# Kernel tuning notes

Measured on AMD Instinct MI355X. Metric: run time of the kernel, lower is better.

Reference implementation:

```python
import jax, jax.numpy as jnp
import numpy as np

N, E, NC = 50000, 800000, 5
H, C = 4, 16      # branch GATConvs: heads=4, out=16 -> 64
H2, C2 = 4, 32    # conv2/conv3: heads=4, out=32 -> 128
HID = 128


def _gat(x, src, dst, W, a_s, a_d, b, mask=None, edge_attr=None, We=None, a_e=None):
    """PyG-style GATConv with add_self_loops=True (fill_value='mean' for edge_attr)."""
    n = x.shape[0]
    h, c = a_s.shape
    hx = (x @ W).reshape(n, h, c)                      # [N,H,C]
    as_n = (hx * a_s).sum(-1)                          # [N,H]
    ad_n = (hx * a_d).sum(-1)                          # [N,H]
    alpha = as_n[src] + ad_n[dst]                      # [E,H]
    loop = as_n + ad_n                                 # self-loop scores [N,H]
    if edge_attr is not None:
        ee = (edge_attr @ We).reshape(-1, h, c)        # [E,H,C]
        alpha = alpha + (ee * a_e).sum(-1)
        w = mask.astype(x.dtype) if mask is not None else jnp.ones((edge_attr.shape[0],), x.dtype)
        # fill_value='mean': self-loop attr = mean of (masked) incoming edge_attr
        loop_attr = jax.ops.segment_sum(edge_attr * w[:, None], dst, n) / \
                    jnp.maximum(jax.ops.segment_sum(w, dst, n), 1.0)[:, None]
        loop = loop + ((loop_attr @ We).reshape(n, h, c) * a_e).sum(-1)
    alpha = jax.nn.leaky_relu(alpha, 0.2)
    loop = jax.nn.leaky_relu(loop, 0.2)
    if mask is not None:
        alpha = jnp.where(mask[:, None], alpha, -jnp.inf)
    # segment softmax over destination neighborhoods (self-loop always present)
    m = jnp.maximum(jax.ops.segment_max(alpha, dst, n), loop)      # [N,H], finite
    ex = jnp.exp(alpha - m[dst])                                   # [E,H]
    if mask is not None:
        ex = jnp.where(mask[:, None], ex, 0.0)
    exl = jnp.exp(loop - m)                                        # [N,H]
    denom = jax.ops.segment_sum(ex, dst, n) + exl
    out = jax.ops.segment_sum(ex[:, :, None] * hx[src], dst, n) + exl[:, :, None] * hx
    return (out / denom[:, :, None]).reshape(n, h * c) + b


def setup_inputs() -> dict:
    key = jax.random.key(0)
    ks = iter(jax.random.split(key, 64))
    def nrm(shape, s=0.1):
        return jax.random.normal(next(ks), shape, jnp.float32) * s
    d = {}
    d["x"] = nrm((N, 1), 1.0)
    d["edge_index"] = jax.random.randint(next(ks), (2, E), 0, N, jnp.int32)
    d["edge_attr"] = nrm((E, 3), 1.0)
    d["mask_t"] = jax.random.randint(next(ks), (E,), 0, 2, jnp.int32).astype(bool)
    d["mask_g"] = jax.random.randint(next(ks), (E,), 0, 2, jnp.int32).astype(bool)
    d["mask_p"] = jax.random.randint(next(ks), (E,), 0, 2, jnp.int32).astype(bool)
    for p in ("t", "g", "p"):
        d[f"W{p}"] = nrm((1, H * C))
        d[f"a{p}s"] = nrm((H, C)); d[f"a{p}d"] = nrm((H, C)); d[f"a{p}e"] = nrm((H, C))
        d[f"W{p}e"] = nrm((3, H * C))
        d[f"b{p}"] = jnp.zeros((H * C,), jnp.float32)
    d["Wf"] = nrm((3 * H * C, HID)); d["bf"] = jnp.zeros((HID,), jnp.float32)
    d["W2"] = nrm((HID, H2 * C2)); d["a2s"] = nrm((H2, C2)); d["a2d"] = nrm((H2, C2)); d["b2"] = jnp.zeros((H2 * C2,), jnp.float32)
    d["W3"] = nrm((HID, H2 * C2)); d["a3s"] = nrm((H2, C2)); d["a3d"] = nrm((H2, C2)); d["b3"] = jnp.zeros((H2 * C2,), jnp.float32)
    d["Wc1"] = nrm((HID, HID // 2)); d["bc1"] = jnp.zeros((HID // 2,), jnp.float32)
    d["Wc2"] = nrm((HID // 2, NC)); d["bc2"] = jnp.zeros((NC,), jnp.float32)
    return d


def reference(x, edge_index, edge_attr, mask_t, mask_g, mask_p,
              Wt, ats, atd, ate, Wte, bt,
              Wg, ags, agd, age, Wge, bg,
              Wp, aps, apd, ape, Wpe, bp,
              Wf, bf, W2, a2s, a2d, b2, W3, a3s, a3d, b3,
              Wc1, bc1, Wc2, bc2):
    src, dst = edge_index[0], edge_index[1]
    ht = _gat(x, src, dst, Wt, ats, atd, bt, mask_t, edge_attr, Wte, ate)
    hg = _gat(x, src, dst, Wg, ags, agd, bg, mask_g, edge_attr, Wge, age)
    hp = _gat(x, src, dst, Wp, aps, apd, bp, mask_p, edge_attr, Wpe, ape)
    h = jax.nn.relu(jnp.concatenate([ht, hg, hp], -1) @ Wf + bf)
    h = jax.nn.relu(_gat(h, src, dst, W2, a2s, a2d, b2))
    h = jax.nn.relu(_gat(h, src, dst, W3, a3s, a3d, b3))
    logits = jax.nn.relu(h @ Wc1 + bc1) @ Wc2 + bc2
    return jax.nn.log_softmax(logits, -1)
```

## Files before the change

kernel.cpp:

```cpp
#include <hip/hip_runtime.h>
#include <hip/hip_bf16.h>

#define LEAKY(v) ((v) > 0.f ? (v) : 0.2f * (v))

typedef __attribute__((ext_vector_type(8))) short s8;
typedef __attribute__((ext_vector_type(4))) float f4;
typedef __attribute__((ext_vector_type(4))) unsigned short us4;

__device__ __forceinline__ unsigned short f_to_bf16(float f) {
    union { float f; unsigned int i; } v; v.f = f;
    unsigned int x = v.i;
    return (unsigned short)((x + 0x7fffu + ((x >> 16) & 1u)) >> 16);
}

__device__ __forceinline__ float2 bf2_to_f2(unsigned int u) {
    union { unsigned int i; float f; } a, b;
    a.i = (u & 0xffffu) << 16;
    b.i = u & 0xffff0000u;
    float2 r; r.x = a.f; r.y = b.f;
    return r;
}

struct ConstBuf {
    float ws[3][4];
    float wd[3][4];
    float M[3][3][4];
    float G[12][128];
    float bias2[128];
};
#define CB_FLOATS 1724

struct BranchW { const float *W, *as_, *ad_, *ae, *We, *b; };
struct PreArgs { BranchW br[3]; const float *Wf, *bf; ConstBuf* cb; };

__global__ void k_pre_all(PreArgs A, const float* __restrict__ W2, unsigned short* __restrict__ wf2,
                          const float* __restrict__ W3, unsigned short* __restrict__ wf3,
                          int* __restrict__ deg, int N) {
    int t = threadIdx.x;
    if (blockIdx.x == 0) {
        if (t < 24) {
            int b = t / 8, r = t % 8, h = r & 3; bool isd = r >= 4;
            const float* a = isd ? A.br[b].ad_ : A.br[b].as_;
            float s = 0.f;
            for (int c = 0; c < 16; ++c) s += A.br[b].W[h * 16 + c] * a[h * 16 + c];
            if (isd) A.cb->wd[b][h] = s; else A.cb->ws[b][h] = s;
        }
        if (t >= 32 && t < 68) {
            int id = t - 32, b = id / 12, k = (id % 12) / 4, h = id & 3;
            float s = 0.f;
            for (int c = 0; c < 16; ++c) s += A.br[b].We[k * 64 + h * 16 + c] * A.br[b].ae[h * 16 + c];
            A.cb->M[b][k][h] = s;
        }
        if (t >= 128) {
            int j = t - 128;
            float s = A.bf[j];
            for (int b = 0; b < 3; ++b)
                for (int i = 0; i < 64; ++i)
                    s += A.br[b].b[i] * A.Wf[(b * 64 + i) * 128 + j];
            A.cb->bias2[j] = s;
        }
        for (int id = t; id < 1536; id += 256) {
            int r = id >> 7, j = id & 127, b = r >> 2, h = r & 3;
            float s = 0.f;
            for (int c = 0; c < 16; ++c)
                s += A.br[b].W[h * 16 + c] * A.Wf[(b * 64 + h * 16 + c) * 128 + j];
            A.cb->G[r][j] = s;
        }
    } else if (blockIdx.x <= 2) {
        const float* W = (blockIdx.x == 1) ? W2 : W3;
        unsigned short* out = (blockIdx.x == 1) ? wf2 : wf3;
        for (int i = t; i < 16384; i += 256) {
            int j = i & 7, lane = (i >> 3) & 63, kk = (i >> 9) & 3, ct = i >> 11;
            int k = kk * 32 + (lane >> 4) * 8 + j;
            int n = ct * 16 + (lane & 15);
            out[i] = f_to_bf16(W[k * 128 + n]);
        }
    } else {
        int idx = (blockIdx.x - 3) * 256 + t;
        if (idx < N) deg[idx] = 0;
    }
}

__global__ void k_count(const int* __restrict__ ei, int E, int* __restrict__ deg) {
    int e = blockIdx.x * blockDim.x + threadIdx.x;
    if (e < E) atomicAdd(&deg[ei[E + e]], 1);
}

#define SCAN_EPB 2048

__global__ void k_scan1(const int* __restrict__ deg, int* __restrict__ off,
                        int* __restrict__ partials, int total) {
    __shared__ int sd[256];
    int t = threadIdx.x;
    int base = blockIdx.x * SCAN_EPB + t * 8;
    int v[8];
    int s = 0;
    #pragma unroll
    for (int i = 0; i < 8; ++i) {
        int idx = base + i;
        v[i] = (idx < total - 1) ? deg[idx] : 0;
        s += v[i];
    }
    sd[t] = s;
    __syncthreads();
    #pragma unroll
    for (int ofs = 1; ofs < 256; ofs <<= 1) {
        int u = (t >= ofs) ? sd[t - ofs] : 0;
        __syncthreads();
        sd[t] += u;
        __syncthreads();
    }
    if (t == 255) partials[blockIdx.x] = sd[255];
    int run = sd[t] - s;
    #pragma unroll
    for (int i = 0; i < 8; ++i) {
        int idx = base + i;
        if (idx < total) off[idx] = run;
        run += v[i];
    }
}

__global__ void k_scan3(int* __restrict__ off, const int* __restrict__ partials,
                        int* __restrict__ cursor, int total) {
    int idx = blockIdx.x * blockDim.x + threadIdx.x;
    if (idx < total) {
        int pb = idx / SCAN_EPB;
        int addv = 0;
        for (int j = 0; j < pb; ++j) addv += partials[j];
        int v = off[idx] + addv;
        off[idx] = v;
        if (idx < total - 1) cursor[idx] = v;
    }
}

__global__ void k_scatter(const int* __restrict__ ei, const float* __restrict__ attr,
                          const int* __restrict__ mt, const int* __restrict__ mg,
                          const int* __restrict__ mp, int E, int chunk,
                          int* __restrict__ cursor, float4* __restrict__ rec) {
    int r = blockIdx.x & 7;
    int slice = blockIdx.x >> 3;
    int e = slice * 256 + threadIdx.x;
    if (e >= E) return;
    int d = ei[E + e];
    if ((unsigned)(d - r * chunk) >= (unsigned)chunk) return;
    int p = atomicAdd(&cursor[d], 1);
    float4 rr;
    rr.x = attr[e * 3 + 0];
    rr.y = attr[e * 3 + 1];
    rr.z = attr[e * 3 + 2];
    unsigned int bits = (mt[e] != 0 ? 1u : 0u) | (mg[e] != 0 ? 2u : 0u) | (mp[e] != 0 ? 4u : 0u);
    rr.w = __int_as_float((int)((unsigned)ei[e] | (bits << 16)));
    rec[p] = rr;
}

__global__ void k_branch(const float* __restrict__ x, const int* __restrict__ off,
                         const float4* __restrict__ rec, int* __restrict__ csr_src,
                         const ConstBuf* __restrict__ cb, float* __restrict__ h1, int N) {
    __shared__ float sc[CB_FLOATS];
    for (int i = threadIdx.x; i < CB_FLOATS; i += 256) sc[i] = ((const float*)cb)[i];
    __syncthreads();
    int g = threadIdx.x >> 4, l = threadIdx.x & 15;
    int n = blockIdx.x * 16 + g;
    if (n >= N) return;

    float num[12], den[12], asum[9], cnt[3];
    #pragma unroll
    for (int i = 0; i < 12; ++i) { num[i] = 0.f; den[i] = 0.f; }
    #pragma unroll
    for (int i = 0; i < 9; ++i) asum[i] = 0.f;
    cnt[0] = cnt[1] = cnt[2] = 0.f;

    float xn = x[n];
    int beg = off[n], end = off[n + 1];
    for (int p = beg + l; p < end; p += 16) {
        float4 r = rec[p];
        unsigned int packed = (unsigned int)__float_as_int(r.w);
        int src = (int)(packed & 0xffffu);
        unsigned int bits = packed >> 16;
        csr_src[p] = src;
        float xs = x[src];
        float a0 = r.x, a1 = r.y, a2 = r.z;
        #pragma unroll
        for (int b = 0; b < 3; ++b) {
            if ((bits >> b) & 1u) {
                cnt[b] += 1.f;
                asum[b * 3 + 0] += a0; asum[b * 3 + 1] += a1; asum[b * 3 + 2] += a2;
                #pragma unroll
                for (int h = 0; h < 4; ++h) {
                    float al = xs * sc[b * 4 + h] + xn * sc[12 + b * 4 + h]
                             + a0 * sc[24 + b * 12 + 0 + h]
                             + a1 * sc[24 + b * 12 + 4 + h]
                             + a2 * sc[24 + b * 12 + 8 + h];
                    al = LEAKY(al);
                    float ex = __expf(al);
                    den[b * 4 + h] += ex;
                    num[b * 4 + h] += ex * xs;
                }
            }
        }
    }
    #pragma unroll
    for (int m = 1; m < 16; m <<= 1) {
        #pragma unroll
        for (int i = 0; i < 12; ++i) {
            num[i] += __shfl_xor(num[i], m, 64);
            den[i] += __shfl_xor(den[i], m, 64);
        }
        #pragma unroll
        for (int i = 0; i < 9; ++i) asum[i] += __shfl_xor(asum[i], m, 64);
        #pragma unroll
        for (int i = 0; i < 3; ++i) cnt[i] += __shfl_xor(cnt[i], m, 64);
    }
    float S[12];
    #pragma unroll
    for (int b = 0; b < 3; ++b) {
        float inv = 1.f / fmaxf(cnt[b], 1.f);
        float l0 = asum[b * 3 + 0] * inv, l1 = asum[b * 3 + 1] * inv, l2 = asum[b * 3 + 2] * inv;
        #pragma unroll
        for (int h = 0; h < 4; ++h) {
            float lp = xn * (sc[b * 4 + h] + sc[12 + b * 4 + h])
                     + l0 * sc[24 + b * 12 + 0 + h]
                     + l1 * sc[24 + b * 12 + 4 + h]
                     + l2 * sc[24 + b * 12 + 8 + h];
            lp = LEAKY(lp);
            float exl = __expf(lp);
            float sden = den[b * 4 + h] + exl;
            S[b * 4 + h] = (num[b * 4 + h] + exl * xn) / sden;
        }
    }
    int jb = l * 8;
    float o[8];
    #pragma unroll
    for (int q = 0; q < 8; ++q) {
        int j = jb + q;
        float a = sc[60 + 1536 + j];
        #pragma unroll
        for (int k = 0; k < 12; ++k) a += S[k] * sc[60 + k * 128 + j];
        o[q] = fmaxf(a, 0.f);
    }
    float4* dst = (float4*)(h1 + (size_t)n * 128 + jb);
    dst[0] = make_float4(o[0], o[1], o[2], o[3]);
    dst[1] = make_float4(o[4], o[5], o[6], o[7]);
}

__global__ void k_mm128b(const float* __restrict__ A, const unsigned short* __restrict__ wf,
                         const float* __restrict__ a_s, const float* __restrict__ a_d,
                         unsigned short* __restrict__ hxb, float* __restrict__ as_,
                         float* __restrict__ ad_, int N) {
    __shared__ unsigned short sA[64 * 136];
    __shared__ unsigned short sW[16384];
    int tid = threadIdx.x;
    int base = blockIdx.x * 64;
    const float4* wf4 = (const float4*)wf;
    float4* sW4 = (float4*)sW;
    #pragma unroll
    for (int i = 0; i < 8; ++i) sW4[tid + i * 256] = wf4[tid + i * 256];
    #pragma unroll
    for (int i = 0; i < 8; ++i) {
        int f = tid + i * 256;
        int row = f >> 5, c4 = f & 31;
        int n = base + row;
        float4 v = (n < N) ? ((const float4*)A)[(size_t)n * 32 + c4]
                           : make_float4(0.f, 0.f, 0.f, 0.f);
        us4 b;
        b.x = f_to_bf16(v.x); b.y = f_to_bf16(v.y);
        b.z = f_to_bf16(v.z); b.w = f_to_bf16(v.w);
        *(us4*)(&sA[row * 136 + c4 * 4]) = b;
    }
    __syncthreads();
    int wv = tid >> 6, lane = tid & 63;
    int q = lane >> 4, l15 = lane & 15;
    int rowbase = wv * 16;
    s8 af[4];
    #pragma unroll
    for (int kk = 0; kk < 4; ++kk)
        af[kk] = *(const s8*)(&sA[(rowbase + l15) * 136 + kk * 32 + q * 8]);
    float as8[8], ad8[8];
    #pragma unroll
    for (int ct = 0; ct < 8; ++ct) { as8[ct] = a_s[ct * 16 + l15]; ad8[ct] = a_d[ct * 16 + l15]; }
    float ss[4][4], sdd[4][4];
    #pragma unroll
    for (int r = 0; r < 4; ++r)
        #pragma unroll
        for (int hh = 0; hh < 4; ++hh) { ss[r][hh] = 0.f; sdd[r][hh] = 0.f; }
    #pragma unroll
    for (int ct = 0; ct < 8; ++ct) {
        f4 acc = {0.f, 0.f, 0.f, 0.f};
        #pragma unroll
        for (int kk = 0; kk < 4; ++kk) {
            s8 bfr = *(const s8*)(&sW[((ct * 4 + kk) * 64 + lane) * 8]);
            acc = __builtin_amdgcn_mfma_f32_16x16x32_bf16(af[kk], bfr, acc, 0, 0, 0);
        }
        int hh = ct >> 1;
        float asv = as8[ct], adv = ad8[ct];
        #pragma unroll
        for (int r = 0; r < 4; ++r) {
            int n = base + rowbase + q * 4 + r;
            if (n < N) hxb[(size_t)n * 128 + ct * 16 + l15] = f_to_bf16(acc[r]);
            ss[r][hh] += acc[r] * asv;
            sdd[r][hh] += acc[r] * adv;
        }
    }
    #pragma unroll
    for (int m = 1; m < 16; m <<= 1) {
        #pragma unroll
        for (int r = 0; r < 4; ++r)
            #pragma unroll
            for (int hh = 0; hh < 4; ++hh) {
                ss[r][hh] += __shfl_xor(ss[r][hh], m, 64);
                sdd[r][hh] += __shfl_xor(sdd[r][hh], m, 64);
            }
    }
    #pragma unroll
    for (int hh = 0; hh < 4; ++hh) {
        if (l15 == hh) {
            #pragma unroll
            for (int r = 0; r < 4; ++r) {
                int n = base + rowbase + q * 4 + r;
                if (n < N) {
                    as_[(size_t)n * 4 + hh] = ss[r][hh];
                    ad_[(size_t)n * 4 + hh] = sdd[r][hh];
                }
            }
        }
    }
}

__global__ void k_gatagg(const unsigned short* __restrict__ hxb, const float* __restrict__ as_,
                         const float* __restrict__ ad_, const float* __restrict__ b,
                         const int* __restrict__ off, const int* __restrict__ csr_src,
                         float* __restrict__ out, int N) {
    int wave = threadIdx.x >> 6, lane = threadIdx.x & 63;
    int n = blockIdx.x * 4 + wave;
    if (n >= N) return;
    int h = lane >> 4;
    int lofs = lane * 2;
    int hm = lane & 3;
    int im = lane >> 2;
    float adn = ad_[(size_t)n * 4 + h];
    float adnm = ad_[(size_t)n * 4 + hm];
    int beg = off[n], end = off[n + 1];
    float acc0 = 0.f, acc1 = 0.f, accd = 0.f;
    for (int p = beg; p < end; p += 16) {
        int pm = p + im;
        bool vm = pm < end;
        int sm = csr_src[vm ? pm : beg];
        float em = as_[(size_t)sm * 4 + hm];
        float exm = vm ? __expf(LEAKY(em + adnm)) : 0.f;
        #pragma unroll
        for (int i = 0; i < 16; ++i) {
            int sb = __shfl(sm, i * 4, 64);
            float ex = __shfl(exm, i * 4 + h, 64);
            unsigned int u = *(const unsigned int*)(hxb + (size_t)sb * 128 + lofs);
            float2 v = bf2_to_f2(u);
            acc0 += ex * v.x; acc1 += ex * v.y; accd += ex;
        }
    }
    float aln = LEAKY(as_[(size_t)n * 4 + h] + adn);
    float exl = __expf(aln);
    unsigned int un = *(const unsigned int*)(hxb + (size_t)n * 128 + lofs);
    float2 vn = bf2_to_f2(un);
    float inv = 1.f / (accd + exl);
    float o0 = (acc0 + exl * vn.x) * inv + b[lofs + 0];
    float o1 = (acc1 + exl * vn.y) * inv + b[lofs + 1];
    float2 r; r.x = fmaxf(o0, 0.f); r.y = fmaxf(o1, 0.f);
    *(float2*)(out + (size_t)n * 128 + lofs) = r;
}

#define CLS_NPB 32
__global__ void k_cls(const float* __restrict__ h3, const float* __restrict__ Wc1,
                      const float* __restrict__ bc1, const float* __restrict__ Wc2,
                      const float* __restrict__ bc2, float* __restrict__ out, int N) {
    __shared__ float hs[CLS_NPB * 128];
    int tid = threadIdx.x;
    int nb = blockIdx.x * CLS_NPB;
    for (int i = tid; i < CLS_NPB * 128; i += 256) {
        int n = nb + (i >> 7);
        hs[i] = (n < N) ? h3[(size_t)n * 128 + (i & 127)] : 0.f;
    }
    __syncthreads();
    int g = tid >> 6, j = tid & 63;
    const float4* hb4 = (const float4*)(hs + g * 8 * 128);
    float bj = bc1[j];
    float acc[8];
    #pragma unroll
    for (int i = 0; i < 8; ++i) acc[i] = bj;
    for (int k = 0; k < 128; k += 4) {
        float w0 = Wc1[(k + 0) * 64 + j];
        float w1 = Wc1[(k + 1) * 64 + j];
        float w2 = Wc1[(k + 2) * 64 + j];
        float w3 = Wc1[(k + 3) * 64 + j];
        #pragma unroll
        for (int i = 0; i < 8; ++i) {
            float4 h4 = hb4[(i * 128 + k) >> 2];
            acc[i] += h4.x * w0 + h4.y * w1 + h4.z * w2 + h4.w * w3;
        }
    }
    float w2v[5];
    #pragma unroll
    for (int c = 0; c < 5; ++c) w2v[c] = Wc2[j * 5 + c];
    #pragma unroll
    for (int i = 0; i < 8; ++i) {
        float t = fmaxf(acc[i], 0.f);
        float p[5];
        #pragma unroll
        for (int c = 0; c < 5; ++c) p[c] = t * w2v[c];
        #pragma unroll
        for (int m = 1; m < 64; m <<= 1) {
            #pragma unroll
            for (int c = 0; c < 5; ++c) p[c] += __shfl_xor(p[c], m, 64);
        }
        if (j == 0) {
            int n = nb + g * 8 + i;
            if (n < N) {
                float l[5], mx = -1e30f;
                #pragma unroll
                for (int c = 0; c < 5; ++c) { l[c] = p[c] + bc2[c]; mx = fmaxf(mx, l[c]); }
                float s = 0.f;
                #pragma unroll
                for (int c = 0; c < 5; ++c) s += __expf(l[c] - mx);
                float lse = mx + __logf(s);
                #pragma unroll
                for (int c = 0; c < 5; ++c) out[(size_t)n * 5 + c] = l[c] - lse;
            }
        }
    }
}

extern "C" void kernel_launch(void* const* d_in, const int* in_sizes, int n_in,
                              void* d_out, int out_size, void* d_ws, size_t ws_size,
                              hipStream_t stream) {
    const float* x    = (const float*)d_in[0];
    const int*   ei   = (const int*)d_in[1];
    const float* attr = (const float*)d_in[2];
    const int*   mt   = (const int*)d_in[3];
    const int*   mg   = (const int*)d_in[4];
    const int*   mp   = (const int*)d_in[5];
    const float* Wf   = (const float*)d_in[24];
    const float* bf   = (const float*)d_in[25];
    const float* W2   = (const float*)d_in[26];
    const float* a2s  = (const float*)d_in[27];
    const float* a2d  = (const float*)d_in[28];
    const float* b2   = (const float*)d_in[29];
    const float* W3   = (const float*)d_in[30];
    const float* a3s  = (const float*)d_in[31];
    const float* a3d  = (const float*)d_in[32];
    const float* b3   = (const float*)d_in[33];
    const float* Wc1  = (const float*)d_in[34];
    const float* bc1  = (const float*)d_in[35];
    const float* Wc2  = (const float*)d_in[36];
    const float* bc2  = (const float*)d_in[37];

    int N = in_sizes[0];
    int E = in_sizes[1] / 2;

    char* w = (char*)d_ws;
    auto alloc = [&](size_t bytes) {
        char* p = w;
        w += (bytes + 255) & ~(size_t)255;
        return p;
    };
    int* off      = (int*)alloc((size_t)(N + 1) * 4);
    int* cursor   = (int*)alloc((size_t)N * 4);
    int* deg      = (int*)alloc((size_t)N * 4);
    int* partials = (int*)alloc(1024 * 4);
    int* csr_src  = (int*)alloc((size_t)E * 4);
    ConstBuf* cb  = (ConstBuf*)alloc(sizeof(ConstBuf));
    float* as_    = (float*)alloc((size_t)N * 4 * 4);
    float* ad_    = (float*)alloc((size_t)N * 4 * 4);
    float* bufA   = (float*)alloc((size_t)N * 128 * 4);
    float4* rec   = (float4*)alloc((size_t)E * 16);
    unsigned short* hxb = (unsigned short*)alloc((size_t)N * 256);
    unsigned short* wf2 = (unsigned short*)alloc(16384 * 2);
    unsigned short* wf3 = (unsigned short*)alloc(16384 * 2);

    PreArgs pa;
    for (int b = 0; b < 3; ++b) {
        pa.br[b].W   = (const float*)d_in[6 + b * 6 + 0];
        pa.br[b].as_ = (const float*)d_in[6 + b * 6 + 1];
        pa.br[b].ad_ = (const float*)d_in[6 + b * 6 + 2];
        pa.br[b].ae  = (const float*)d_in[6 + b * 6 + 3];
        pa.br[b].We  = (const float*)d_in[6 + b * 6 + 4];
        pa.br[b].b   = (const float*)d_in[6 + b * 6 + 5];
    }
    pa.Wf = Wf; pa.bf = bf; pa.cb = cb;

    int total = N + 1;
    int nScanBlocks = (total + SCAN_EPB - 1) / SCAN_EPB;

    hipLaunchKernelGGL(k_pre_all, dim3(3 + (N + 255) / 256), dim3(256), 0, stream,
                       pa, W2, wf2, W3, wf3, deg, N);
    int gE = (E + 255) / 256;
    hipLaunchKernelGGL(k_count, dim3(gE), dim3(256), 0, stream, ei, E, deg);
    hipLaunchKernelGGL(k_scan1, dim3(nScanBlocks), dim3(256), 0, stream, deg, off, partials, total);
    hipLaunchKernelGGL(k_scan3, dim3((total + 255) / 256), dim3(256), 0, stream,
                       off, partials, cursor, total);
    int chunk = (N + 7) / 8;
    hipLaunchKernelGGL(k_scatter, dim3(gE * 8), dim3(256), 0, stream,
                       ei, attr, mt, mg, mp, E, chunk, cursor, rec);
    hipLaunchKernelGGL(k_branch, dim3((N + 15) / 16), dim3(256), 0, stream,
                       x, off, rec, csr_src, cb, bufA, N);
    hipLaunchKernelGGL(k_mm128b, dim3((N + 63) / 64), dim3(256), 0, stream,
                       bufA, wf2, a2s, a2d, hxb, as_, ad_, N);
    hipLaunchKernelGGL(k_gatagg, dim3((N + 3) / 4), dim3(256), 0, stream,
                       hxb, as_, ad_, b2, off, csr_src, bufA, N);
    hipLaunchKernelGGL(k_mm128b, dim3((N + 63) / 64), dim3(256), 0, stream,
                       bufA, wf3, a3s, a3d, hxb, as_, ad_, N);
    hipLaunchKernelGGL(k_gatagg, dim3((N + 3) / 4), dim3(256), 0, stream,
                       hxb, as_, ad_, b3, off, csr_src, bufA, N);
    hipLaunchKernelGGL(k_cls, dim3((N + CLS_NPB - 1) / CLS_NPB), dim3(256), 0, stream,
                       bufA, Wc1, bc1, Wc2, bc2, (float*)d_out, N);
}
```

Measured before the change: 438.4 us.

## Store intermediate node features in bf16 and run classifier on MFMA

Intermediate 128-wide node features from the branch, GAT aggregation and classifier input are now written and read as bf16 instead of fp32. This halves their memory traffic and removes the fp32-to-bf16 conversion inside the matmul loader. The classifier's first layer now uses bf16 MFMA with a weight matrix pre-swizzled in the prep kernel, replacing the scalar FMA loop. The cost is lower precision in the stored activations and in the classifier matmul.

Measured after the change: 403.8 us (median of 2 runs). 7.9% less time.

```diff
diff --git a/kernel.cpp b/kernel.cpp
--- a/kernel.cpp
+++ b/kernel.cpp
@@ -35,6 +35,7 @@
 
 __global__ void k_pre_all(PreArgs A, const float* __restrict__ W2, unsigned short* __restrict__ wf2,
                           const float* __restrict__ W3, unsigned short* __restrict__ wf3,
+                          const float* __restrict__ Wc1, unsigned short* __restrict__ wc1f,
                           int* __restrict__ deg, int N) {
     int t = threadIdx.x;
     if (blockIdx.x == 0) {
@@ -75,8 +76,15 @@
             int n = ct * 16 + (lane & 15);
             out[i] = f_to_bf16(W[k * 128 + n]);
         }
+    } else if (blockIdx.x == 3) {
+        for (int i = t; i < 8192; i += 256) {
+            int j = i & 7, lane = (i >> 3) & 63, kk = (i >> 9) & 3, ct = i >> 11;
+            int k = kk * 32 + (lane >> 4) * 8 + j;
+            int col = ct * 16 + (lane & 15);
+            wc1f[i] = f_to_bf16(Wc1[k * 64 + col]);
+        }
     } else {
-        int idx = (blockIdx.x - 3) * 256 + t;
+        int idx = (blockIdx.x - 4) * 256 + t;
         if (idx < N) deg[idx] = 0;
     }
 }
@@ -155,7 +163,7 @@
 
 __global__ void k_branch(const float* __restrict__ x, const int* __restrict__ off,
                          const float4* __restrict__ rec, int* __restrict__ csr_src,
-                         const ConstBuf* __restrict__ cb, float* __restrict__ h1, int N) {
+                         const ConstBuf* __restrict__ cb, unsigned short* __restrict__ h1, int N) {
     __shared__ float sc[CB_FLOATS];
     for (int i = threadIdx.x; i < CB_FLOATS; i += 256) sc[i] = ((const float*)cb)[i];
     __syncthreads();
@@ -229,21 +237,25 @@
         }
     }
     int jb = l * 8;
-    float o[8];
-    #pragma unroll
-    for (int q = 0; q < 8; ++q) {
-        int j = jb + q;
-        float a = sc[60 + 1536 + j];
-        #pragma unroll
-        for (int k = 0; k < 12; ++k) a += S[k] * sc[60 + k * 128 + j];
-        o[q] = fmaxf(a, 0.f);
-    }
-    float4* dst = (float4*)(h1 + (size_t)n * 128 + jb);
-    dst[0] = make_float4(o[0], o[1], o[2], o[3]);
-    dst[1] = make_float4(o[4], o[5], o[6], o[7]);
-}
-
-__global__ void k_mm128b(const float* __restrict__ A, const unsigned short* __restrict__ wf,
+    unsigned int o[4];
+    #pragma unroll
+    for (int q2 = 0; q2 < 4; ++q2) {
+        float v0, v1;
+        #pragma unroll
+        for (int s = 0; s < 2; ++s) {
+            int j = jb + q2 * 2 + s;
+            float a = sc[60 + 1536 + j];
+            #pragma unroll
+            for (int k = 0; k < 12; ++k) a += S[k] * sc[60 + k * 128 + j];
+            if (s == 0) v0 = fmaxf(a, 0.f); else v1 = fmaxf(a, 0.f);
+        }
+        o[q2] = (unsigned int)f_to_bf16(v0) | ((unsigned int)f_to_bf16(v1) << 16);
+    }
+    uint4 pack; pack.x = o[0]; pack.y = o[1]; pack.z = o[2]; pack.w = o[3];
+    *(uint4*)(h1 + (size_t)n * 128 + jb) = pack;
+}
+
+__global__ void k_mm128b(const unsigned short* __restrict__ A, const unsigned short* __restrict__ wf,
                          const float* __restrict__ a_s, const float* __restrict__ a_d,
                          unsigned short* __restrict__ hxb, float* __restrict__ as_,
                          float* __restrict__ ad_, int N) {
@@ -256,16 +268,13 @@
     #pragma unroll
     for (int i = 0; i < 8; ++i) sW4[tid + i * 256] = wf4[tid + i * 256];
     #pragma unroll
-    for (int i = 0; i < 8; ++i) {
+    for (int i = 0; i < 4; ++i) {
         int f = tid + i * 256;
-        int row = f >> 5, c4 = f & 31;
+        int row = f >> 4, c8 = f & 15;
         int n = base + row;
-        float4 v = (n < N) ? ((const float4*)A)[(size_t)n * 32 + c4]
-                           : make_float4(0.f, 0.f, 0.f, 0.f);
-        us4 b;
-        b.x = f_to_bf16(v.x); b.y = f_to_bf16(v.y);
-        b.z = f_to_bf16(v.z); b.w = f_to_bf16(v.w);
-        *(us4*)(&sA[row * 136 + c4 * 4]) = b;
+        uint4 v = (n < N) ? ((const uint4*)A)[(size_t)n * 16 + c8]
+                          : make_uint4(0u, 0u, 0u, 0u);
+        *(uint4*)(&sA[row * 136 + c8 * 8]) = v;
     }
     __syncthreads();
     int wv = tid >> 6, lane = tid & 63;
@@ -329,7 +338,7 @@
 __global__ void k_gatagg(const unsigned short* __restrict__ hxb, const float* __restrict__ as_,
                          const float* __restrict__ ad_, const float* __restrict__ b,
                          const int* __restrict__ off, const int* __restrict__ csr_src,
-                         float* __restrict__ out, int N) {
+                         unsigned short* __restrict__ out, int N) {
     int wave = threadIdx.x >> 6, lane = threadIdx.x & 63;
     int n = blockIdx.x * 4 + wave;
     if (n >= N) return;
@@ -361,68 +370,87 @@
     unsigned int un = *(const unsigned int*)(hxb + (size_t)n * 128 + lofs);
     float2 vn = bf2_to_f2(un);
     float inv = 1.f / (accd + exl);
-    float o0 = (acc0 + exl * vn.x) * inv + b[lofs + 0];
-    float o1 = (acc1 + exl * vn.y) * inv + b[lofs + 1];
-    float2 r; r.x = fmaxf(o0, 0.f); r.y = fmaxf(o1, 0.f);
-    *(float2*)(out + (size_t)n * 128 + lofs) = r;
-}
-
-#define CLS_NPB 32
-__global__ void k_cls(const float* __restrict__ h3, const float* __restrict__ Wc1,
+    float o0 = fmaxf((acc0 + exl * vn.x) * inv + b[lofs + 0], 0.f);
+    float o1 = fmaxf((acc1 + exl * vn.y) * inv + b[lofs + 1], 0.f);
+    unsigned int pk = (unsigned int)f_to_bf16(o0) | ((unsigned int)f_to_bf16(o1) << 16);
+    *(unsigned int*)(out + (size_t)n * 128 + lofs) = pk;
+}
+
+__global__ void k_cls(const unsigned short* __restrict__ h3, const unsigned short* __restrict__ wc1f,
                       const float* __restrict__ bc1, const float* __restrict__ Wc2,
                       const float* __restrict__ bc2, float* __restrict__ out, int N) {
-    __shared__ float hs[CLS_NPB * 128];
+    __shared__ unsigned short sA[64 * 136];
+    __shared__ unsigned short sW[8192];
     int tid = threadIdx.x;
-    int nb = blockIdx.x * CLS_NPB;
-    for (int i = tid; i < CLS_NPB * 128; i += 256) {
-        int n = nb + (i >> 7);
-        hs[i] = (n < N) ? h3[(size_t)n * 128 + (i & 127)] : 0.f;
+    int base = blockIdx.x * 64;
+    const float4* wf4 = (const float4*)wc1f;
+    float4* sW4 = (float4*)sW;
+    #pragma unroll
+    for (int i = 0; i < 4; ++i) sW4[tid + i * 256] = wf4[tid + i * 256];
+    #pragma unroll
+    for (int i = 0; i < 4; ++i) {
+        int f = tid + i * 256;
+        int row = f >> 4, c8 = f & 15;
+        int n = base + row;
+        uint4 v = (n < N) ? ((const uint4*)h3)[(size_t)n * 16 + c8]
+                          : make_uint4(0u, 0u, 0u, 0u);
+        *(uint4*)(&sA[row * 136 + c8 * 8]) = v;
     }
     __syncthreads();
-    int g = tid >> 6, j = tid & 63;
-    const float4* hb4 = (const float4*)(hs + g * 8 * 128);
-    float bj = bc1[j];
-    float acc[8];
-    #pragma unroll
-    for (int i = 0; i < 8; ++i) acc[i] = bj;
-    for (int k = 0; k < 128; k += 4) {
-        float w0 = Wc1[(k + 0) * 64 + j];
-        float w1 = Wc1[(k + 1) * 64 + j];
-        float w2 = Wc1[(k + 2) * 64 + j];
-        float w3 = Wc1[(k + 3) * 64 + j];
-        #pragma unroll
-        for (int i = 0; i < 8; ++i) {
-            float4 h4 = hb4[(i * 128 + k) >> 2];
-            acc[i] += h4.x * w0 + h4.y * w1 + h4.z * w2 + h4.w * w3;
-        }
-    }
-    float w2v[5];
-    #pragma unroll
-    for (int c = 0; c < 5; ++c) w2v[c] = Wc2[j * 5 + c];
-    #pragma unroll
-    for (int i = 0; i < 8; ++i) {
-        float t = fmaxf(acc[i], 0.f);
-        float p[5];
-        #pragma unroll
-        for (int c = 0; c < 5; ++c) p[c] = t * w2v[c];
-        #pragma unroll
-        for (int m = 1; m < 64; m <<= 1) {
-            #pragma unroll
-            for (int c = 0; c < 5; ++c) p[c] += __shfl_xor(p[c], m, 64);
-        }
-        if (j == 0) {
-            int n = nb + g * 8 + i;
-            if (n < N) {
-                float l[5], mx = -1e30f;
-                #pragma unroll
-                for (int c = 0; c < 5; ++c) { l[c] = p[c] + bc2[c]; mx = fmaxf(mx, l[c]); }
-                float s = 0.f;
-                #pragma unroll
-                for (int c = 0; c < 5; ++c) s += __expf(l[c] - mx);
-                float lse = mx + __logf(s);
-                #pragma unroll
-                for (int c = 0; c < 5; ++c) out[(size_t)n * 5 + c] = l[c] - lse;
-            }
+    int wv = tid >> 6, lane = tid & 63;
+    int q = lane >> 4, l15 = lane & 15;
+    int rowbase = wv * 16;
+    s8 af[4];
+    #pragma unroll
+    for (int kk = 0; kk < 4; ++kk)
+        af[kk] = *(const s8*)(&sA[(rowbase + l15) * 136 + kk * 32 + q * 8]);
+    float p[4][5];
+    #pragma unroll
+    for (int r = 0; r < 4; ++r)
+        #pragma unroll
+        for (int c = 0; c < 5; ++c) p[r][c] = 0.f;
+    #pragma unroll
+    for (int ct = 0; ct < 4; ++ct) {
+        f4 acc = {0.f, 0.f, 0.f, 0.f};
+        #pragma unroll
+        for (int kk = 0; kk < 4; ++kk) {
+            s8 bfr = *(const s8*)(&sW[((ct * 4 + kk) * 64 + lane) * 8]);
+            acc = __builtin_amdgcn_mfma_f32_16x16x32_bf16(af[kk], bfr, acc, 0, 0, 0);
+        }
+        int col = ct * 16 + l15;
+        float bcv = bc1[col];
+        float w2v[5];
+        #pragma unroll
+        for (int c = 0; c < 5; ++c) w2v[c] = Wc2[col * 5 + c];
+        #pragma unroll
+        for (int r = 0; r < 4; ++r) {
+            float t = fmaxf(acc[r] + bcv, 0.f);
+            #pragma unroll
+            for (int c = 0; c < 5; ++c) p[r][c] += t * w2v[c];
+        }
+    }
+    #pragma unroll
+    for (int m = 1; m < 16; m <<= 1) {
+        #pragma unroll
+        for (int r = 0; r < 4; ++r)
+            #pragma unroll
+            for (int c = 0; c < 5; ++c)
+                p[r][c] += __shfl_xor(p[r][c], m, 64);
+    }
+    if (l15 == 0) {
+        #pragma unroll
+        for (int r = 0; r < 4; ++r) {
+            int n = base + rowbase + q * 4 + r;
+            if (n >= N) continue;
+            float l[5], mx = -1e30f;
+            #pragma unroll
+            for (int c = 0; c < 5; ++c) { l[c] = p[r][c] + bc2[c]; mx = fmaxf(mx, l[c]); }
+            float s = 0.f;
+            #pragma unroll
+            for (int c = 0; c < 5; ++c) s += __expf(l[c] - mx);
+            float lse = mx + __logf(s);
+            #pragma unroll
+            for (int c = 0; c < 5; ++c) out[(size_t)n * 5 + c] = l[c] - lse;
         }
     }
 }
@@ -468,11 +496,12 @@
     ConstBuf* cb  = (ConstBuf*)alloc(sizeof(ConstBuf));
     float* as_    = (float*)alloc((size_t)N * 4 * 4);
     float* ad_    = (float*)alloc((size_t)N * 4 * 4);
-    float* bufA   = (float*)alloc((size_t)N * 128 * 4);
+    unsigned short* xb = (unsigned short*)alloc((size_t)N * 256);
     float4* rec   = (float4*)alloc((size_t)E * 16);
     unsigned short* hxb = (unsigned short*)alloc((size_t)N * 256);
     unsigned short* wf2 = (unsigned short*)alloc(16384 * 2);
     unsigned short* wf3 = (unsigned short*)alloc(16384 * 2);
+    unsigned short* wc1f = (unsigned short*)alloc(8192 * 2);
 
     PreArgs pa;
     for (int b = 0; b < 3; ++b) {
@@ -488,8 +517,8 @@
     int total = N + 1;
     int nScanBlocks = (total + SCAN_EPB - 1) / SCAN_EPB;
 
-    hipLaunchKernelGGL(k_pre_all, dim3(3 + (N + 255) / 256), dim3(256), 0, stream,
-                       pa, W2, wf2, W3, wf3, deg, N);
+    hipLaunchKernelGGL(k_pre_all, dim3(4 + (N + 255) / 256), dim3(256), 0, stream,
+                       pa, W2, wf2, W3, wf3, Wc1, wc1f, deg, N);
     int gE = (E + 255) / 256;
     hipLaunchKernelGGL(k_count, dim3(gE), dim3(256), 0, stream, ei, E, deg);
     hipLaunchKernelGGL(k_scan1, dim3(nScanBlocks), dim3(256), 0, stream, deg, off, partials, total);
@@ -499,15 +528,15 @@
     hipLaunchKernelGGL(k_scatter, dim3(gE * 8), dim3(256), 0, stream,
                        ei, attr, mt, mg, mp, E, chunk, cursor, rec);
     hipLaunchKernelGGL(k_branch, dim3((N + 15) / 16), dim3(256), 0, stream,
-                       x, off, rec, csr_src, cb, bufA, N);
+                       x, off, rec, csr_src, cb, xb, N);
     hipLaunchKernelGGL(k_mm128b, dim3((N + 63) / 64), dim3(256), 0, stream,
-                       bufA, wf2, a2s, a2d, hxb, as_, ad_, N);
+                       xb, wf2, a2s, a2d, hxb, as_, ad_, N);
     hipLaunchKernelGGL(k_gatagg, dim3((N + 3) / 4), dim3(256), 0, stream,
-                       hxb, as_, ad_, b2, off, csr_src, bufA, N);
+                       hxb, as_, ad_, b2, off, csr_src, xb, N);
     hipLaunchKernelGGL(k_mm128b, dim3((N + 63) / 64), dim3(256), 0, stream,
-                       bufA, wf3, a3s, a3d, hxb, as_, ad_, N);
+                       xb, wf3, a3s, a3d, hxb, as_, ad_, N);
     hipLaunchKernelGGL(k_gatagg, dim3((N + 3) / 4), dim3(256), 0, stream,
-                       hxb, as_, ad_, b3, off, csr_src, bufA, N);
-    hipLaunchKernelGGL(k_cls, dim3((N + CLS_NPB - 1) / CLS_NPB), dim3(256), 0, stream,
-                       bufA, Wc1, bc1, Wc2, bc2, (float*)d_out, N);
-}
+                       hxb, as_, ad_, b3, off, csr_src, xb, N);
+    hipLaunchKernelGGL(k_cls, dim3((N + 63) / 64), dim3(256), 0, stream,
+                       xb, wc1f, bc1, Wc2, bc2, (float*)d_out, N);
+}
```
